# Performance work log

Measured on AMD Instinct MI355X. Metric: run time of the kernel, lower is better.

Reference implementation:

```python
import jax, jax.numpy as jnp
import numpy as np
from jax import lax

XI = 2.0
RADIUS = int(3 * XI)  # 6 -> kernel size 13


def _gaussian_weight(xi: float):
    radius = int(3 * xi)
    coords = jnp.arange(-radius, radius + 1, dtype=jnp.float32)
    g1 = jnp.exp(-coords ** 2 / (2.0 * xi * xi))
    g1 = g1 / g1.sum()
    g3 = g1[:, None, None] * g1[None, :, None] * g1[None, None, :]  # (K,K,K)
    # grouped conv weight: (out_ch=3, in_ch/groups=1, K, K, K), same kernel per channel
    return jnp.broadcast_to(g3[None, None], (3, 1) + g3.shape)


def setup_inputs() -> dict:
    key = jax.random.key(0)
    x = jax.random.normal(key, (1, 3, 192, 192, 192), dtype=jnp.float32)
    w = _gaussian_weight(XI)
    return {"x": x, "w": w}


def reference(x, w):
    # depthwise (groups=3) 3D cross-correlation with 'same' padding = radius,
    # matching nn.Conv3d(3, 3, (K,K,K), padding=radius, groups=3, bias=False)
    r = (w.shape[-1] - 1) // 2
    return lax.conv_general_dilated(
        x, w,
        window_strides=(1, 1, 1),
        padding=[(r, r)] * 3,
        dimension_numbers=("NCDHW", "OIDHW", "NCDHW"),
        feature_group_count=3,
    )
```

## Files before the change

### kernel.cpp

```cpp
#include <hip/hip_runtime.h>

#define RAD 6
#define KS 13
#define DIM 192
#define CH 3
#define W4C (DIM / 4)
#define VOL (DIM * DIM * DIM)
#define TOTAL (CH * VOL)

__global__ void g1_extract_kernel(const float* __restrict__ w, float* __restrict__ g1) {
    int i = threadIdx.x;
    if (i < KS) {
        float s = 0.f;
        for (int j = 0; j < KS * KS; ++j) s += w[i * KS * KS + j];
        g1[i] = s;
    }
}

__global__ __launch_bounds__(256) void conv_w_kernel(const float* __restrict__ in,
                                                     float* __restrict__ out,
                                                     const float* __restrict__ g1) {
    int q = blockIdx.x * 256 + threadIdx.x;
    float g[KS];
#pragma unroll
    for (int k = 0; k < KS; ++k) g[k] = g1[k];

    int w4 = q % W4C;
    int w0 = w4 * 4;
    const float4* in4 = (const float4*)in;

    float f[20];
#pragma unroll
    for (int b = 0; b < 5; ++b) {
        int idx = q + b - 2;
        idx = min(max(idx, 0), TOTAL / 4 - 1);
        float4 v = in4[idx];
        f[4 * b + 0] = v.x; f[4 * b + 1] = v.y;
        f[4 * b + 2] = v.z; f[4 * b + 3] = v.w;
    }
#pragma unroll
    for (int j = 0; j < 20; ++j) {
        int ww = w0 - 8 + j;
        if (ww < 0 || ww >= DIM) f[j] = 0.f;
    }

    float4 o; o.x = o.y = o.z = o.w = 0.f;
#pragma unroll
    for (int k = 0; k < KS; ++k) {
        o.x += g[k] * f[k + 2];
        o.y += g[k] * f[k + 3];
        o.z += g[k] * f[k + 4];
        o.w += g[k] * f[k + 5];
    }
    ((float4*)out)[q] = o;
}

template <int AX4, int OT4>
__global__ __launch_bounds__(256) void conv_col_kernel(const float* __restrict__ in,
                                                       float* __restrict__ out,
                                                       const float* __restrict__ g1) {
    const int COLS = CH * DIM * W4C;
    const int SEGS = 8;
    const int L = DIM / SEGS;
    int t = blockIdx.x * 256 + threadIdx.x;
    int seg = t / COLS;
    int colid = t % COLS;
    int c = colid / (DIM * W4C);
    int rem = colid % (DIM * W4C);
    int other = rem / W4C;
    int w4 = rem % W4C;
    size_t base4 = (size_t)c * (VOL / 4) + (size_t)other * OT4 + (size_t)w4;

    const float4* in4 = (const float4*)in;
    float4* out4 = (float4*)out;

    float g[KS];
#pragma unroll
    for (int k = 0; k < KS; ++k) g[k] = g1[k];

    const float4 z4 = make_float4(0.f, 0.f, 0.f, 0.f);
    int d0 = seg * L;

    float4 buf[KS];
#pragma unroll
    for (int j = 0; j < KS; ++j) {
        int dd = d0 - RAD + j;
        buf[j] = (dd >= 0 && dd < DIM) ? in4[base4 + (size_t)dd * AX4] : z4;
    }

    int d = d0;
    auto body = [&](int s) {
        int dl = d + RAD + 1;
        float4 nv = (dl < DIM) ? in4[base4 + (size_t)dl * AX4] : z4;
        float4 a; a.x = a.y = a.z = a.w = 0.f;
#pragma unroll
        for (int j = 0; j < KS; ++j) {
            const float4 v = buf[(s + j) % KS];
            float gw = g[j];
            a.x += gw * v.x; a.y += gw * v.y; a.z += gw * v.z; a.w += gw * v.w;
        }
        out4[base4 + (size_t)d * AX4] = a;
        buf[s] = nv;
        ++d;
    };

#pragma unroll
    for (int s = 0; s < KS; ++s) body(s);
#pragma unroll
    for (int s = 0; s < 11; ++s) body(s);
}

__global__ void naive_conv3d_kernel(const float* __restrict__ x, const float* __restrict__ w,
                                    float* __restrict__ out, int total) {
    int n = blockIdx.x * blockDim.x + threadIdx.x;
    if (n >= total) return;
    int wp = n % DIM;
    int h = (n / DIM) % DIM;
    int d = (n / (DIM * DIM)) % DIM;
    int c = n / (DIM * DIM * DIM);
    const float* wc = w + c * KS * KS * KS;
    const float* xc = x + (size_t)c * DIM * DIM * DIM;
    float acc = 0.f;
    for (int kd = 0; kd < KS; ++kd) {
        int dd = d + kd - RAD;
        if (dd < 0 || dd >= DIM) continue;
        for (int kh = 0; kh < KS; ++kh) {
            int hh = h + kh - RAD;
            if (hh < 0 || hh >= DIM) continue;
            for (int kw = 0; kw < KS; ++kw) {
                int ww = wp + kw - RAD;
                if (ww < 0 || ww >= DIM) continue;
                acc += wc[(kd * KS + kh) * KS + kw] * xc[((size_t)dd * DIM + hh) * DIM + ww];
            }
        }
    }
    out[n] = acc;
}

extern "C" void kernel_launch(void* const* d_in, const int* in_sizes, int n_in,
                              void* d_out, int out_size, void* d_ws, size_t ws_size,
                              hipStream_t stream) {
    const float* x = (const float*)d_in[0];
    const float* w = (const float*)d_in[1];
    float* out = (float*)d_out;

    const size_t inter_bytes = (size_t)TOTAL * sizeof(float);

    if (ws_size >= inter_bytes + 64) {
        float* inter = (float*)d_ws;
        float* g1 = (float*)((char*)d_ws + inter_bytes);

        g1_extract_kernel<<<1, 64, 0, stream>>>(w, g1);

        conv_w_kernel<<<TOTAL / 4 / 256, 256, 0, stream>>>(x, out, g1);

        conv_col_kernel<DIM / 4, DIM * DIM / 4>
            <<<(8 * CH * DIM * W4C) / 256, 256, 0, stream>>>(out, inter, g1);

        conv_col_kernel<DIM * DIM / 4, DIM / 4>
            <<<(8 * CH * DIM * W4C) / 256, 256, 0, stream>>>(inter, out, g1);
    } else {
        const int threads = 256;
        const int blocks = (TOTAL + threads - 1) / threads;
        naive_conv3d_kernel<<<blocks, threads, 0, stream>>>(x, w, out, TOTAL);
    }
}
```

Measured before the change: 211.1 us.

## Fuse W and H separable passes via shared-memory tile; tile D pass in LDS

Merges the W-axis and H-axis 1D Gaussian passes into one kernel. Each block loads a 64-row slab of a D-plane plus halo into shared memory, applies the W pass in place, then applies the H pass from LDS. This removes one full intermediate write and read of the volume. The D pass now stages a 192x16-float4 column tile in LDS before convolving. In exchange, halo rows are recomputed, large per-thread register arrays and LDS use may cut occupancy, and the grid is only 1728 blocks.

```diff
diff --git a/kernel.cpp b/kernel.cpp
--- a/kernel.cpp
+++ b/kernel.cpp
@@ -4,7 +4,9 @@
 #define KS 13
 #define DIM 192
 #define CH 3
-#define W4C (DIM / 4)
+#define W4C 48
+#define PLANE4 (DIM * W4C)
+#define VOL4 (DIM * PLANE4)
 #define VOL (DIM * DIM * DIM)
 #define TOTAL (CH * VOL)
 
@@ -17,97 +19,158 @@
     }
 }
 
-__global__ __launch_bounds__(256) void conv_w_kernel(const float* __restrict__ in,
+#define HT 64
+#define HL (HT + 2 * RAD)
+#define NLD (HL * W4C)
+
+__global__ __launch_bounds__(256) void conv_wh_kernel(const float* __restrict__ in,
+                                                      float* __restrict__ out,
+                                                      const float* __restrict__ g1) {
+    __shared__ float4 tile[NLD];
+    const int bid = blockIdx.x;
+    const int ht = bid % 3;
+    const int d = (bid / 3) % DIM;
+    const int c = bid / (3 * DIM);
+    const int h0 = ht * HT;
+    const int t = threadIdx.x;
+
+    float g[KS];
+#pragma unroll
+    for (int k = 0; k < KS; ++k) g[k] = g1[k];
+
+    const float4* in4 = (const float4*)in;
+    float4* out4 = (float4*)out;
+    const size_t plane = (size_t)c * VOL4 + (size_t)d * PLANE4;
+    const float4 z4 = make_float4(0.f, 0.f, 0.f, 0.f);
+
+#pragma unroll
+    for (int i = 0; i < 15; ++i) {
+        int idx = t + i * 256;
+        if (idx < NLD) {
+            int h = h0 - RAD + idx / W4C;
+            tile[idx] = (h >= 0 && h < DIM) ? in4[plane + (size_t)h * W4C + (idx % W4C)] : z4;
+        }
+    }
+    __syncthreads();
+
+    float4 va[15];
+#pragma unroll
+    for (int i = 0; i < 15; ++i) {
+        int idx = t + i * 256;
+        if (idx < NLD) {
+            int row = idx / W4C, w4 = idx % W4C;
+            int w0 = w4 * 4;
+            float f[20];
+#pragma unroll
+            for (int b = 0; b < 5; ++b) {
+                int j = min(max(w4 + b - 2, 0), W4C - 1);
+                float4 v = tile[row * W4C + j];
+                f[4 * b + 0] = v.x; f[4 * b + 1] = v.y;
+                f[4 * b + 2] = v.z; f[4 * b + 3] = v.w;
+            }
+#pragma unroll
+            for (int j = 0; j < 20; ++j) {
+                int ww = w0 - 8 + j;
+                if (ww < 0 || ww >= DIM) f[j] = 0.f;
+            }
+            float4 o = z4;
+#pragma unroll
+            for (int k = 0; k < KS; ++k) {
+                o.x += g[k] * f[k + 2];
+                o.y += g[k] * f[k + 3];
+                o.z += g[k] * f[k + 4];
+                o.w += g[k] * f[k + 5];
+            }
+            va[i] = o;
+        }
+    }
+    __syncthreads();
+#pragma unroll
+    for (int i = 0; i < 15; ++i) {
+        int idx = t + i * 256;
+        if (idx < NLD) tile[idx] = va[i];
+    }
+    __syncthreads();
+
+    if (t < 192) {
+        int w4 = t % W4C;
+        int seg = t / W4C;
+        int hh0 = seg * 16;
+
+        float4 buf[KS];
+#pragma unroll
+        for (int j = 0; j < KS; ++j) buf[j] = tile[(hh0 + j) * W4C + w4];
+
+#pragma unroll
+        for (int i = 0; i < 16; ++i) {
+            float4 a = z4;
+#pragma unroll
+            for (int j = 0; j < KS; ++j) {
+                const float4 v = buf[(i + j) % KS];
+                float gw = g[j];
+                a.x += gw * v.x; a.y += gw * v.y; a.z += gw * v.z; a.w += gw * v.w;
+            }
+            out4[plane + (size_t)(h0 + hh0 + i) * W4C + w4] = a;
+            if (i < 15) buf[i % KS] = tile[(hh0 + i + KS) * W4C + w4];
+        }
+    }
+}
+
+#define WT 16
+
+__global__ __launch_bounds__(256) void conv_d_kernel(const float* __restrict__ in,
                                                      float* __restrict__ out,
                                                      const float* __restrict__ g1) {
-    int q = blockIdx.x * 256 + threadIdx.x;
+    __shared__ float4 tile[DIM * WT];
+    const int bid = blockIdx.x;
+    const int wt = bid % 3;
+    const int h = (bid / 3) % DIM;
+    const int c = bid / (3 * DIM);
+    const int t = threadIdx.x;
+
     float g[KS];
 #pragma unroll
     for (int k = 0; k < KS; ++k) g[k] = g1[k];
-
-    int w4 = q % W4C;
-    int w0 = w4 * 4;
-    const float4* in4 = (const float4*)in;
-
-    float f[20];
-#pragma unroll
-    for (int b = 0; b < 5; ++b) {
-        int idx = q + b - 2;
-        idx = min(max(idx, 0), TOTAL / 4 - 1);
-        float4 v = in4[idx];
-        f[4 * b + 0] = v.x; f[4 * b + 1] = v.y;
-        f[4 * b + 2] = v.z; f[4 * b + 3] = v.w;
-    }
-#pragma unroll
-    for (int j = 0; j < 20; ++j) {
-        int ww = w0 - 8 + j;
-        if (ww < 0 || ww >= DIM) f[j] = 0.f;
-    }
-
-    float4 o; o.x = o.y = o.z = o.w = 0.f;
-#pragma unroll
-    for (int k = 0; k < KS; ++k) {
-        o.x += g[k] * f[k + 2];
-        o.y += g[k] * f[k + 3];
-        o.z += g[k] * f[k + 4];
-        o.w += g[k] * f[k + 5];
-    }
-    ((float4*)out)[q] = o;
-}
-
-template <int AX4, int OT4>
-__global__ __launch_bounds__(256) void conv_col_kernel(const float* __restrict__ in,
-                                                       float* __restrict__ out,
-                                                       const float* __restrict__ g1) {
-    const int COLS = CH * DIM * W4C;
-    const int SEGS = 8;
-    const int L = DIM / SEGS;
-    int t = blockIdx.x * 256 + threadIdx.x;
-    int seg = t / COLS;
-    int colid = t % COLS;
-    int c = colid / (DIM * W4C);
-    int rem = colid % (DIM * W4C);
-    int other = rem / W4C;
-    int w4 = rem % W4C;
-    size_t base4 = (size_t)c * (VOL / 4) + (size_t)other * OT4 + (size_t)w4;
 
     const float4* in4 = (const float4*)in;
     float4* out4 = (float4*)out;
-
-    float g[KS];
-#pragma unroll
-    for (int k = 0; k < KS; ++k) g[k] = g1[k];
-
+    const size_t base = (size_t)c * VOL4 + (size_t)h * W4C + wt * WT;
     const float4 z4 = make_float4(0.f, 0.f, 0.f, 0.f);
-    int d0 = seg * L;
+
+#pragma unroll
+    for (int i = 0; i < 12; ++i) {
+        int idx = t + i * 256;
+        int dd = idx / WT, w = idx % WT;
+        tile[idx] = in4[base + (size_t)dd * PLANE4 + w];
+    }
+    __syncthreads();
+
+    int w = t % WT;
+    int seg = t / WT;
+    int d0 = seg * 12;
 
     float4 buf[KS];
 #pragma unroll
     for (int j = 0; j < KS; ++j) {
         int dd = d0 - RAD + j;
-        buf[j] = (dd >= 0 && dd < DIM) ? in4[base4 + (size_t)dd * AX4] : z4;
-    }
-
-    int d = d0;
-    auto body = [&](int s) {
-        int dl = d + RAD + 1;
-        float4 nv = (dl < DIM) ? in4[base4 + (size_t)dl * AX4] : z4;
-        float4 a; a.x = a.y = a.z = a.w = 0.f;
+        buf[j] = (dd >= 0 && dd < DIM) ? tile[dd * WT + w] : z4;
+    }
+
+#pragma unroll
+    for (int i = 0; i < 12; ++i) {
+        float4 a = z4;
 #pragma unroll
         for (int j = 0; j < KS; ++j) {
-            const float4 v = buf[(s + j) % KS];
+            const float4 v = buf[(i + j) % KS];
             float gw = g[j];
             a.x += gw * v.x; a.y += gw * v.y; a.z += gw * v.z; a.w += gw * v.w;
         }
-        out4[base4 + (size_t)d * AX4] = a;
-        buf[s] = nv;
-        ++d;
-    };
-
-#pragma unroll
-    for (int s = 0; s < KS; ++s) body(s);
-#pragma unroll
-    for (int s = 0; s < 11; ++s) body(s);
+        out4[base + (size_t)(d0 + i) * PLANE4 + w] = a;
+        if (i < 11) {
+            int dl = d0 + i + RAD + 1;
+            buf[i % KS] = (dl < DIM) ? tile[dl * WT + w] : z4;
+        }
+    }
 }
 
 __global__ void naive_conv3d_kernel(const float* __restrict__ x, const float* __restrict__ w,
@@ -152,13 +215,9 @@
 
         g1_extract_kernel<<<1, 64, 0, stream>>>(w, g1);
 
-        conv_w_kernel<<<TOTAL / 4 / 256, 256, 0, stream>>>(x, out, g1);
-
-        conv_col_kernel<DIM / 4, DIM * DIM / 4>
-            <<<(8 * CH * DIM * W4C) / 256, 256, 0, stream>>>(out, inter, g1);
-
-        conv_col_kernel<DIM * DIM / 4, DIM / 4>
-            <<<(8 * CH * DIM * W4C) / 256, 256, 0, stream>>>(inter, out, g1);
+        conv_wh_kernel<<<CH * DIM * 3, 256, 0, stream>>>(x, inter, g1);
+
+        conv_d_kernel<<<CH * DIM * 3, 256, 0, stream>>>(inter, out, g1);
     } else {
         const int threads = 256;
         const int blocks = (TOTAL + threads - 1) / threads;
```

Result: no change. 213.7 us (+1.3%).
